# Kernel optimization log

Hardware: AMD Instinct MI355X
Metric: run time of the kernel (lower is better)

Reference implementation:

```python
import jax, jax.numpy as jnp
import numpy as np

HEADS = 8
DIM_HEAD = 64
WINDOW = 128
PERSIST = 4
EPS = 1.1920929e-07  # torch nn.RMSNorm default eps = finfo(fp32).eps


def _rope_freqs(n, d, dtype):
    inv_freq = 1.0 / (10000.0 ** (jnp.arange(0, d, 2, dtype=jnp.float32) / d))
    freqs = jnp.arange(n, dtype=jnp.float32)[:, None] * inv_freq[None, :]  # [n, d/2]
    freqs = jnp.repeat(freqs, 2, axis=-1)  # interleaved repeat -> [n, d]
    return jnp.cos(freqs).astype(dtype), jnp.sin(freqs).astype(dtype)


def _rotate_half(x):
    # interleaved pairs (x0,x1),(x2,x3)... -> (-x1,x0),(-x3,x2)...
    x = x.reshape(*x.shape[:-1], -1, 2)
    x1, x2 = x[..., 0], x[..., 1]
    return jnp.stack((-x2, x1), axis=-1).reshape(*x.shape[:-2], -1)


def setup_inputs() -> dict:
    key = jax.random.key(0)
    k1, k2, k3 = jax.random.split(key, 3)
    B, N, D = 1, 4096, 1024
    dim_inner = HEADS * DIM_HEAD  # 512
    return {
        "seq": jax.random.normal(k1, (B, N, D), dtype=jnp.float32),
        "g": jnp.ones((D,), dtype=jnp.float32),
        "w_qkv": jax.random.normal(k2, (D, 3 * dim_inner), dtype=jnp.float32) * 0.02,
        "w_out": jax.random.normal(k3, (dim_inner, D), dtype=jnp.float32) * 0.02,
    }


def reference(seq, g, w_qkv, w_out):
    B, N, D = seq.shape
    H, Dh = HEADS, DIM_HEAD

    # RMSNorm
    x = seq * jax.lax.rsqrt(jnp.mean(seq * seq, axis=-1, keepdims=True) + EPS) * g

    # QKV projection -> [B, H, N, Dh]
    qkv = x @ w_qkv
    q, k, v = jnp.split(qkv, 3, axis=-1)
    to_heads = lambda t: t.reshape(B, N, H, Dh).transpose(0, 2, 1, 3)
    q, k, v = map(to_heads, (q, k, v))

    # rotary embeddings (same positions for q and k)
    cos, sin = _rope_freqs(N, Dh, q.dtype)
    q = q * cos + _rotate_half(q) * sin
    k = k * cos + _rotate_half(k) * sin

    # causal & (persist | sliding-window) mask
    idx = jnp.arange(N)
    dist = idx[:, None] - idx[None, :]
    mask = (dist >= 0) & ((idx[None, :] < PERSIST) | (dist <= WINDOW))  # [N, N]

    scale = Dh ** -0.5
    scores = jnp.einsum("bhid,bhjd->bhij", q, k) * scale
    neg = -jnp.finfo(scores.dtype).max
    scores = jnp.where(mask[None, None], scores, neg)
    attn = jax.nn.softmax(scores, axis=-1)
    out = jnp.einsum("bhij,bhjd->bhid", attn, v)

    out = out.transpose(0, 2, 1, 3).reshape(B, N, H * Dh)
    return out @ w_out
```

## Files before the change

### kernel.cpp

```cpp
#include <hip/hip_runtime.h>
#include <hip/hip_bf16.h>
#include <math.h>

#define SEQ    4096
#define DMODEL 1024
#define NHEADS 8
#define DH     64
#define DINNER 512
#define NQKV   1536
#define WINDOW 128
#define PERSIST 4
#define EPS 1.1920929e-07f

typedef unsigned short u16;
typedef unsigned int   u32;
typedef __bf16  bf16_8 __attribute__((ext_vector_type(8)));
typedef float   f32x4  __attribute__((ext_vector_type(4)));

union BV { bf16_8 v; u16 s[8]; };

__device__ __forceinline__ float b2f(u16 u) {
    union { u32 i; float f; } v; v.i = ((u32)u) << 16; return v.f;
}
__device__ __forceinline__ u16 f2b(float f) {
    union { float f; u32 i; } v; v.f = f;
    u32 i = v.i;
    u32 r = (i + 0x7fffu + ((i >> 16) & 1u)) >> 16;
    return (u16)r;
}

#define GLD16(gp, lp) __builtin_amdgcn_global_load_lds( \
    (const __attribute__((address_space(1))) void*)(gp), \
    (__attribute__((address_space(3))) void*)(lp), 16, 0, 0)

__device__ __forceinline__ void transpose_tile(const float* __restrict__ src,
                                               u16* __restrict__ dst,
                                               int K, int N, int bn, int bk,
                                               u16 (*t)[65], int tid) {
    int r = tid >> 4, c4 = (tid & 15) * 4;
    #pragma unroll
    for (int it = 0; it < 4; it++) {
        int row = r + it * 16;
        float4 v = *(const float4*)(src + (size_t)(bk + row) * N + bn + c4);
        t[row][c4 + 0] = f2b(v.x);
        t[row][c4 + 1] = f2b(v.y);
        t[row][c4 + 2] = f2b(v.z);
        t[row][c4 + 3] = f2b(v.w);
    }
    __syncthreads();
    #pragma unroll
    for (int it = 0; it < 4; it++) {
        int n = r + it * 16;
        u16* d = dst + (size_t)(bn + n) * K + bk + c4;
        d[0] = t[c4 + 0][n];
        d[1] = t[c4 + 1][n];
        d[2] = t[c4 + 2][n];
        d[3] = t[c4 + 3][n];
    }
}

__global__ __launch_bounds__(256) void prep_kernel(const float* __restrict__ wqkv,
                                                   const float* __restrict__ wout,
                                                   const float* __restrict__ seq,
                                                   const float* __restrict__ g,
                                                   u16* __restrict__ wqkv_bt,
                                                   u16* __restrict__ wout_bt,
                                                   u16* __restrict__ x) {
    __shared__ u16 t[64][65];
    __shared__ float wsum[4];
    int b = blockIdx.x, tid = threadIdx.x;
    if (b < 384) {
        transpose_tile(wqkv, wqkv_bt, DMODEL, NQKV, (b % 24) * 64, (b / 24) * 64, t, tid);
    } else if (b < 512) {
        int bb = b - 384;
        transpose_tile(wout, wout_bt, DINNER, DMODEL, (bb % 16) * 64, (bb / 16) * 64, t, tid);
    } else {
        int row = b - 512;
        float4 v = *(const float4*)(seq + (size_t)row * DMODEL + tid * 4);
        float ss = v.x*v.x + v.y*v.y + v.z*v.z + v.w*v.w;
        #pragma unroll
        for (int o = 32; o > 0; o >>= 1) ss += __shfl_xor(ss, o);
        if ((tid & 63) == 0) wsum[tid >> 6] = ss;
        __syncthreads();
        float tot = wsum[0] + wsum[1] + wsum[2] + wsum[3];
        float rstd = rsqrtf(tot * (1.0f / DMODEL) + EPS);
        float4 gv = *(const float4*)(g + tid * 4);
        uint2 o;
        o.x = (u32)f2b(v.x * rstd * gv.x) | ((u32)f2b(v.y * rstd * gv.y) << 16);
        o.y = (u32)f2b(v.z * rstd * gv.z) | ((u32)f2b(v.w * rstd * gv.w) << 16);
        *(uint2*)(x + (size_t)row * DMODEL + tid * 4) = o;
    }
}

template <int MODE, int NTW>
__global__ __launch_bounds__(256, 2) void gemm2_kernel(const u16* __restrict__ A,
                                                       const u16* __restrict__ Bt,
                                                       u16* __restrict__ C0,
                                                       u16* __restrict__ C1,
                                                       u16* __restrict__ C2,
                                                       float* __restrict__ Cf,
                                                       int M, int N, int K) {
    constexpr int BN  = NTW * 32;
    constexpr int GPW = BN / 32;
    __shared__ u16 As[128 * 64];
    __shared__ u16 Bs[BN * 64];
    int bx = blockIdx.x, by = blockIdx.y, tid = threadIdx.x;
    int lane = tid & 63, wave = tid >> 6;
    int m16 = lane & 15, quad = lane >> 4;
    int rw0 = (wave & 1) * 64, cw0 = (wave >> 1) * (NTW * 16);

    f32x4 acc[4][NTW];
    #pragma unroll
    for (int mt = 0; mt < 4; mt++)
        #pragma unroll
        for (int nt = 0; nt < NTW; nt++) acc[mt][nt] = (f32x4){0.f, 0.f, 0.f, 0.f};

    int lrow = lane & 7, lkc = lane >> 3;
    const u16* Ag = A  + (size_t)(by * 128 + lrow) * K + lkc * 8;
    const u16* Bg = Bt + (size_t)(bx * BN  + lrow) * K + lkc * 8;

    for (int k0 = 0; k0 < K; k0 += 64) {
        #pragma unroll
        for (int r = 0; r < 4; r++) {
            int gg = wave * 4 + r;
            GLD16(Ag + (size_t)(gg * 8) * K + k0, As + gg * 512);
        }
        #pragma unroll
        for (int r = 0; r < GPW; r++) {
            int gg = wave * GPW + r;
            GLD16(Bg + (size_t)(gg * 8) * K + k0, Bs + gg * 512);
        }
        __syncthreads();

        #pragma unroll
        for (int kk = 0; kk < 2; kk++) {
            int kc = kk * 4 + quad;
            bf16_8 afr[4], bfr[NTW];
            #pragma unroll
            for (int mt = 0; mt < 4; mt++) {
                int row = rw0 + mt * 16 + m16;
                afr[mt] = *(const bf16_8*)(As + (row >> 3) * 512 + kc * 64 + (row & 7) * 8);
            }
            #pragma unroll
            for (int nt = 0; nt < NTW; nt++) {
                int col = cw0 + nt * 16 + m16;
                bfr[nt] = *(const bf16_8*)(Bs + (col >> 3) * 512 + kc * 64 + (col & 7) * 8);
            }
            #pragma unroll
            for (int mt = 0; mt < 4; mt++)
                #pragma unroll
                for (int nt = 0; nt < NTW; nt++)
                    acc[mt][nt] = __builtin_amdgcn_mfma_f32_16x16x32_bf16(afr[mt], bfr[nt], acc[mt][nt], 0, 0, 0);
        }
        __syncthreads();
    }

    #pragma unroll
    for (int nt = 0; nt < NTW; nt++) {
        int col = bx * BN + cw0 + nt * 16 + m16;
        if (MODE == 0) {
            int tt = (col & 63) >> 1;
            float inv = exp2f(-(float)(2 * tt) * (13.287712379549449f / 64.0f));
            bool isv = (col >= 2 * DINNER);
            bool odd = (col & 1);
            int tens = col >> 9, hh = (col >> 6) & 7, dh = col & 63;
            u16* dst = (tens == 0) ? C0 : ((tens == 1) ? C1 : C2);
            #pragma unroll
            for (int mt = 0; mt < 4; mt++) {
                #pragma unroll
                for (int r = 0; r < 4; r++) {
                    int row = by * 128 + rw0 + mt * 16 + quad * 4 + r;
                    float own = acc[mt][nt][r];
                    float part = __shfl_xor(own, 1);
                    float val = own;
                    if (!isv) {
                        float s, c;
                        __sincosf((float)row * inv, &s, &c);
                        val = odd ? (own * c + part * s) : (own * c - part * s);
                    }
                    dst[((size_t)hh * SEQ + row) * DH + dh] = f2b(val);
                }
            }
        } else {
            #pragma unroll
            for (int mt = 0; mt < 4; mt++) {
                #pragma unroll
                for (int r = 0; r < 4; r++) {
                    int row = by * 128 + rw0 + mt * 16 + quad * 4 + r;
                    Cf[(size_t)row * N + col] = acc[mt][nt][r];
                }
            }
        }
    }
}

#define AROWS 208
#define KLD   72
#define PLD   168
#define VLD   222

__global__ __launch_bounds__(256, 2) void attn_mfma(const u16* __restrict__ Q,
                                                    const u16* __restrict__ Kt,
                                                    const u16* __restrict__ V,
                                                    u16* __restrict__ O) {
    __shared__ __align__(16) char smem[29952 + 64 * VLD * 2];
    u16* Ks = (u16*)smem;
    u16* Ps = (u16*)smem;
    u16* Vt = (u16*)(smem + 29952);
    int i0 = blockIdx.x * 64, h = blockIdx.y;
    int tid = threadIdx.x, wave = tid >> 6, lane = tid & 63;
    int m16 = lane & 15, quad = lane >> 4;
    int smin = (i0 > WINDOW) ? i0 - WINDOW : 0;

    for (int idx = tid; idx < AROWS * 8; idx += 256) {
        int row = idx >> 3, c = idx & 7;
        int j = (row < 16) ? row : (smin + row - 16);
        size_t goff = ((size_t)h * SEQ + j) * DH + c * 8;
        *(bf16_8*)(Ks + row * KLD + c * 8) = *(const bf16_8*)(Kt + goff);
        union BV u; u.v = *(const bf16_8*)(V + goff);
        #pragma unroll
        for (int e = 0; e < 8; e++) Vt[(c * 8 + e) * VLD + row] = u.s[e];
    }

    int iw0 = i0 + wave * 16;
    int iq = iw0 + m16;
    const u16* qrow = Q + ((size_t)h * SEQ + iq) * DH;
    bf16_8 qa = *(const bf16_8*)(qrow + quad * 8);
    bf16_8 qb = *(const bf16_8*)(qrow + 32 + quad * 8);
    __syncthreads();

    int start_w = (iw0 > WINDOW) ? iw0 - WINDOW : 0;
    int Dw = start_w - smin;
    int tlast = 31 + iw0 - start_w;
    int nch = (tlast >> 4) + 1;
    int nk32 = (tlast >> 5) + 1;

    f32x4 S[10];
    __builtin_amdgcn_s_setprio(1);
    #pragma unroll
    for (int c = 0; c < 10; c++) {
        if (c < nch) {
            int t = c * 16 + m16;
            int row = (c == 0) ? t : (t + Dw);
            const u16* kp = Ks + row * KLD;
            bf16_8 kb0 = *(const bf16_8*)(kp + quad * 8);
            bf16_8 kb1 = *(const bf16_8*)(kp + 32 + quad * 8);
            f32x4 s = (f32x4){0.f, 0.f, 0.f, 0.f};
            s = __builtin_amdgcn_mfma_f32_16x16x32_bf16(qa, kb0, s, 0, 0, 0);
            s = __builtin_amdgcn_mfma_f32_16x16x32_bf16(qb, kb1, s, 0, 0, 0);
            S[c] = s;
        }
    }
    __builtin_amdgcn_s_setprio(0);
    __syncthreads();

    float mrow[4] = {-1e30f, -1e30f, -1e30f, -1e30f};
    #pragma unroll
    for (int c = 0; c < 10; c++) {
        if (c < nch) {
            int t = c * 16 + m16;
            int j = (c == 0) ? t : (start_w + t - 16);
            #pragma unroll
            for (int r = 0; r < 4; r++) {
                int i = iw0 + quad * 4 + r;
                bool valid = (c == 0) ? (j < PERSIST && j < start_w)
                                      : (j <= i && (i - j <= WINDOW || j < PERSIST));
                float sv = valid ? S[c][r] * 0.125f : -1e30f;
                S[c][r] = sv;
                mrow[r] = fmaxf(mrow[r], sv);
            }
        }
    }
    #pragma unroll
    for (int r = 0; r < 4; r++) {
        #pragma unroll
        for (int o = 1; o < 16; o <<= 1) mrow[r] = fmaxf(mrow[r], __shfl_xor(mrow[r], o));
    }
    float srow[4] = {0.f, 0.f, 0.f, 0.f};
    #pragma unroll
    for (int c = 0; c < 10; c++) {
        if (c < nch) {
            #pragma unroll
            for (int r = 0; r < 4; r++) {
                float p = __expf(S[c][r] - mrow[r]);
                S[c][r] = p;
                srow[r] += p;
            }
        }
    }
    #pragma unroll
    for (int r = 0; r < 4; r++) {
        #pragma unroll
        for (int o = 1; o < 16; o <<= 1) srow[r] += __shfl_xor(srow[r], o);
    }

    u16* pw = Ps + wave * 16 * PLD;
    #pragma unroll
    for (int c = 0; c < 10; c++) {
        #pragma unroll
        for (int r = 0; r < 4; r++) {
            u16 val = (c < nch) ? f2b(S[c][r]) : (u16)0;
            pw[(quad * 4 + r) * PLD + c * 16 + m16] = val;
        }
    }

    f32x4 oacc[4];
    #pragma unroll
    for (int nt = 0; nt < 4; nt++) oacc[nt] = (f32x4){0.f, 0.f, 0.f, 0.f};
    __builtin_amdgcn_s_setprio(1);
    #pragma unroll
    for (int c2 = 0; c2 < 5; c2++) {
        if (c2 < nk32) {
            bf16_8 af = *(const bf16_8*)(pw + m16 * PLD + c2 * 32 + quad * 8);
            int kbase = c2 * 32 + quad * 8;
            int rowb = (kbase < 16) ? kbase : (kbase + Dw);
            #pragma unroll
            for (int nt = 0; nt < 4; nt++) {
                int d = nt * 16 + m16;
                bf16_8 bv = *(const bf16_8*)(Vt + d * VLD + rowb);
                oacc[nt] = __builtin_amdgcn_mfma_f32_16x16x32_bf16(af, bv, oacc[nt], 0, 0, 0);
            }
        }
    }
    __builtin_amdgcn_s_setprio(0);

    float rinv[4];
    #pragma unroll
    for (int r = 0; r < 4; r++) rinv[r] = 1.0f / srow[r];
    #pragma unroll
    for (int nt = 0; nt < 4; nt++) {
        #pragma unroll
        for (int r = 0; r < 4; r++) {
            int i = iw0 + quad * 4 + r;
            O[(size_t)i * DINNER + h * DH + nt * 16 + m16] = f2b(oacc[nt][r] * rinv[r]);
        }
    }
}

extern "C" void kernel_launch(void* const* d_in, const int* in_sizes, int n_in,
                              void* d_out, int out_size, void* d_ws, size_t ws_size,
                              hipStream_t stream) {
    const float* seq  = (const float*)d_in[0];
    const float* g    = (const float*)d_in[1];
    const float* wqkv = (const float*)d_in[2];
    const float* wout = (const float*)d_in[3];
    float* out = (float*)d_out;

    char* ws = (char*)d_ws;
    u16* x       = (u16*)(ws);
    u16* q       = (u16*)(ws + 8ll  * 1024 * 1024);
    u16* k       = (u16*)(ws + 12ll * 1024 * 1024);
    u16* v       = (u16*)(ws + 16ll * 1024 * 1024);
    u16* att     = (u16*)(ws + 20ll * 1024 * 1024);
    u16* wqkv_bt = (u16*)(ws + 24ll * 1024 * 1024);
    u16* wout_bt = (u16*)(ws + 27ll * 1024 * 1024);

    prep_kernel<<<4608, 256, 0, stream>>>(wqkv, wout, seq, g, wqkv_bt, wout_bt, x);

    dim3 g1(NQKV / 96, SEQ / 128);
    gemm2_kernel<0, 3><<<g1, 256, 0, stream>>>(x, wqkv_bt, q, k, v, nullptr, SEQ, NQKV, DMODEL);

    dim3 g2(SEQ / 64, NHEADS);
    attn_mfma<<<g2, 256, 0, stream>>>(q, k, v, att);

    dim3 g3(DMODEL / 64, SEQ / 128);
    gemm2_kernel<1, 2><<<g3, 256, 0, stream>>>(att, wout_bt, nullptr, nullptr, nullptr, out, SEQ, DMODEL, DINNER);
}
```

Baseline: 141.0 us.

## Store V transposed from QKV GEMM, widen GEMM K-step, vectorize transpose stores

```diff
diff --git a/kernel.cpp b/kernel.cpp
--- a/kernel.cpp
+++ b/kernel.cpp
@@ -52,10 +52,10 @@
     for (int it = 0; it < 4; it++) {
         int n = r + it * 16;
         u16* d = dst + (size_t)(bn + n) * K + bk + c4;
-        d[0] = t[c4 + 0][n];
-        d[1] = t[c4 + 1][n];
-        d[2] = t[c4 + 2][n];
-        d[3] = t[c4 + 3][n];
+        uint2 o;
+        o.x = (u32)t[c4 + 0][n] | ((u32)t[c4 + 1][n] << 16);
+        o.y = (u32)t[c4 + 2][n] | ((u32)t[c4 + 3][n] << 16);
+        *(uint2*)d = o;
     }
 }
 
@@ -92,7 +92,7 @@
     }
 }
 
-template <int MODE, int NTW>
+template <int MODE, int NTW, int KTOT>
 __global__ __launch_bounds__(256, 2) void gemm2_kernel(const u16* __restrict__ A,
                                                        const u16* __restrict__ Bt,
                                                        u16* __restrict__ C0,
@@ -102,8 +102,8 @@
                                                        int M, int N, int K) {
     constexpr int BN  = NTW * 32;
     constexpr int GPW = BN / 32;
-    __shared__ u16 As[128 * 64];
-    __shared__ u16 Bs[BN * 64];
+    __shared__ u16 As[2][128 * 64];
+    __shared__ u16 Bs[2][BN * 64];
     int bx = blockIdx.x, by = blockIdx.y, tid = threadIdx.x;
     int lane = tid & 63, wave = tid >> 6;
     int m16 = lane & 15, quad = lane >> 4;
@@ -116,41 +116,47 @@
         for (int nt = 0; nt < NTW; nt++) acc[mt][nt] = (f32x4){0.f, 0.f, 0.f, 0.f};
 
     int lrow = lane & 7, lkc = lane >> 3;
-    const u16* Ag = A  + (size_t)(by * 128 + lrow) * K + lkc * 8;
-    const u16* Bg = Bt + (size_t)(bx * BN  + lrow) * K + lkc * 8;
-
-    for (int k0 = 0; k0 < K; k0 += 64) {
-        #pragma unroll
-        for (int r = 0; r < 4; r++) {
-            int gg = wave * 4 + r;
-            GLD16(Ag + (size_t)(gg * 8) * K + k0, As + gg * 512);
-        }
-        #pragma unroll
-        for (int r = 0; r < GPW; r++) {
-            int gg = wave * GPW + r;
-            GLD16(Bg + (size_t)(gg * 8) * K + k0, Bs + gg * 512);
+    const u16* Ag = A  + (size_t)(by * 128 + lrow) * KTOT + lkc * 8;
+    const u16* Bg = Bt + (size_t)(bx * BN  + lrow) * KTOT + lkc * 8;
+
+    for (int k0 = 0; k0 < KTOT; k0 += 128) {
+        #pragma unroll
+        for (int hb = 0; hb < 2; hb++) {
+            #pragma unroll
+            for (int r = 0; r < 4; r++) {
+                int gg = wave * 4 + r;
+                GLD16(Ag + (size_t)(gg * 8) * KTOT + k0 + hb * 64, As[hb] + gg * 512);
+            }
+            #pragma unroll
+            for (int r = 0; r < GPW; r++) {
+                int gg = wave * GPW + r;
+                GLD16(Bg + (size_t)(gg * 8) * KTOT + k0 + hb * 64, Bs[hb] + gg * 512);
+            }
         }
         __syncthreads();
 
         #pragma unroll
-        for (int kk = 0; kk < 2; kk++) {
-            int kc = kk * 4 + quad;
-            bf16_8 afr[4], bfr[NTW];
-            #pragma unroll
-            for (int mt = 0; mt < 4; mt++) {
-                int row = rw0 + mt * 16 + m16;
-                afr[mt] = *(const bf16_8*)(As + (row >> 3) * 512 + kc * 64 + (row & 7) * 8);
-            }
-            #pragma unroll
-            for (int nt = 0; nt < NTW; nt++) {
-                int col = cw0 + nt * 16 + m16;
-                bfr[nt] = *(const bf16_8*)(Bs + (col >> 3) * 512 + kc * 64 + (col & 7) * 8);
-            }
-            #pragma unroll
-            for (int mt = 0; mt < 4; mt++)
-                #pragma unroll
-                for (int nt = 0; nt < NTW; nt++)
-                    acc[mt][nt] = __builtin_amdgcn_mfma_f32_16x16x32_bf16(afr[mt], bfr[nt], acc[mt][nt], 0, 0, 0);
+        for (int hb = 0; hb < 2; hb++) {
+            #pragma unroll
+            for (int kk = 0; kk < 2; kk++) {
+                int kc = kk * 4 + quad;
+                bf16_8 afr[4], bfr[NTW];
+                #pragma unroll
+                for (int mt = 0; mt < 4; mt++) {
+                    int row = rw0 + mt * 16 + m16;
+                    afr[mt] = *(const bf16_8*)(As[hb] + (row >> 3) * 512 + kc * 64 + (row & 7) * 8);
+                }
+                #pragma unroll
+                for (int nt = 0; nt < NTW; nt++) {
+                    int col = cw0 + nt * 16 + m16;
+                    bfr[nt] = *(const bf16_8*)(Bs[hb] + (col >> 3) * 512 + kc * 64 + (col & 7) * 8);
+                }
+                #pragma unroll
+                for (int mt = 0; mt < 4; mt++)
+                    #pragma unroll
+                    for (int nt = 0; nt < NTW; nt++)
+                        acc[mt][nt] = __builtin_amdgcn_mfma_f32_16x16x32_bf16(afr[mt], bfr[nt], acc[mt][nt], 0, 0, 0);
+            }
         }
         __syncthreads();
     }
@@ -159,26 +165,33 @@
     for (int nt = 0; nt < NTW; nt++) {
         int col = bx * BN + cw0 + nt * 16 + m16;
         if (MODE == 0) {
-            int tt = (col & 63) >> 1;
-            float inv = exp2f(-(float)(2 * tt) * (13.287712379549449f / 64.0f));
-            bool isv = (col >= 2 * DINNER);
-            bool odd = (col & 1);
             int tens = col >> 9, hh = (col >> 6) & 7, dh = col & 63;
-            u16* dst = (tens == 0) ? C0 : ((tens == 1) ? C1 : C2);
-            #pragma unroll
-            for (int mt = 0; mt < 4; mt++) {
-                #pragma unroll
-                for (int r = 0; r < 4; r++) {
-                    int row = by * 128 + rw0 + mt * 16 + quad * 4 + r;
-                    float own = acc[mt][nt][r];
-                    float part = __shfl_xor(own, 1);
-                    float val = own;
-                    if (!isv) {
+            if (tens == 2) {
+                #pragma unroll
+                for (int mt = 0; mt < 4; mt++) {
+                    int nb = by * 128 + rw0 + mt * 16 + quad * 4;
+                    uint2 o;
+                    o.x = (u32)f2b(acc[mt][nt][0]) | ((u32)f2b(acc[mt][nt][1]) << 16);
+                    o.y = (u32)f2b(acc[mt][nt][2]) | ((u32)f2b(acc[mt][nt][3]) << 16);
+                    *(uint2*)(C2 + ((size_t)(hh * DH + dh)) * SEQ + nb) = o;
+                }
+            } else {
+                int tt = (col & 63) >> 1;
+                float inv = exp2f(-(float)(2 * tt) * (13.287712379549449f / 64.0f));
+                bool odd = (col & 1);
+                u16* dst = (tens == 0) ? C0 : C1;
+                #pragma unroll
+                for (int mt = 0; mt < 4; mt++) {
+                    #pragma unroll
+                    for (int r = 0; r < 4; r++) {
+                        int row = by * 128 + rw0 + mt * 16 + quad * 4 + r;
+                        float own = acc[mt][nt][r];
+                        float part = __shfl_xor(own, 1);
                         float s, c;
                         __sincosf((float)row * inv, &s, &c);
-                        val = odd ? (own * c + part * s) : (own * c - part * s);
+                        float val = odd ? (own * c + part * s) : (own * c - part * s);
+                        dst[((size_t)hh * SEQ + row) * DH + dh] = f2b(val);
                     }
-                    dst[((size_t)hh * SEQ + row) * DH + dh] = f2b(val);
                 }
             }
         } else {
@@ -201,7 +214,7 @@
 
 __global__ __launch_bounds__(256, 2) void attn_mfma(const u16* __restrict__ Q,
                                                     const u16* __restrict__ Kt,
-                                                    const u16* __restrict__ V,
+                                                    const u16* __restrict__ Vg,
                                                     u16* __restrict__ O) {
     __shared__ __align__(16) char smem[29952 + 64 * VLD * 2];
     u16* Ks = (u16*)smem;
@@ -215,11 +228,15 @@
     for (int idx = tid; idx < AROWS * 8; idx += 256) {
         int row = idx >> 3, c = idx & 7;
         int j = (row < 16) ? row : (smin + row - 16);
-        size_t goff = ((size_t)h * SEQ + j) * DH + c * 8;
-        *(bf16_8*)(Ks + row * KLD + c * 8) = *(const bf16_8*)(Kt + goff);
-        union BV u; u.v = *(const bf16_8*)(V + goff);
-        #pragma unroll
-        for (int e = 0; e < 8; e++) Vt[(c * 8 + e) * VLD + row] = u.s[e];
+        *(bf16_8*)(Ks + row * KLD + c * 8) =
+            *(const bf16_8*)(Kt + ((size_t)h * SEQ + j) * DH + c * 8);
+    }
+    for (int idx = tid; idx < 64 * 26; idx += 256) {
+        int d = idx / 26, c = idx - d * 26;
+        int t0 = c * 8;
+        int n0 = (c < 2) ? t0 : (smin + t0 - 16);
+        *(bf16_8*)(Vt + d * VLD + t0) =
+            *(const bf16_8*)(Vg + ((size_t)(h * DH + d)) * SEQ + n0);
     }
 
     int iw0 = i0 + wave * 16;
@@ -358,11 +375,11 @@
     prep_kernel<<<4608, 256, 0, stream>>>(wqkv, wout, seq, g, wqkv_bt, wout_bt, x);
 
     dim3 g1(NQKV / 96, SEQ / 128);
-    gemm2_kernel<0, 3><<<g1, 256, 0, stream>>>(x, wqkv_bt, q, k, v, nullptr, SEQ, NQKV, DMODEL);
+    gemm2_kernel<0, 3, DMODEL><<<g1, 256, 0, stream>>>(x, wqkv_bt, q, k, v, nullptr, SEQ, NQKV, DMODEL);
 
     dim3 g2(SEQ / 64, NHEADS);
     attn_mfma<<<g2, 256, 0, stream>>>(q, k, v, att);
 
     dim3 g3(DMODEL / 64, SEQ / 128);
-    gemm2_kernel<1, 2><<<g3, 256, 0, stream>>>(att, wout_bt, nullptr, nullptr, nullptr, out, SEQ, DMODEL, DINNER);
-}
+    gemm2_kernel<1, 2, DINNER><<<g3, 256, 0, stream>>>(att, wout_bt, nullptr, nullptr, nullptr, out, SEQ, DMODEL, DINNER);
+}
```

After: 140.6 us. Within noise of the previous version (-0.3%).
